# Kernel optimization log

Hardware: AMD Instinct MI355X
Metric: run time of the kernel (lower is better)

Reference implementation:

```python
import jax, jax.numpy as jnp
import numpy as np

B, IN_DIM, OUT_DIM, DEGREE = 4096, 1024, 1024, 4
LN_EPS = 1e-5


def setup_inputs() -> dict:
    key = jax.random.key(0)
    k_x, k_c = jax.random.split(key)
    x = jax.random.normal(k_x, (B, IN_DIM), dtype=jnp.float32)
    # xavier_normal_ on tensor of shape (in, out, deg+1): fan_in/fan_out from
    # torch convention: fan_in = out*(deg+1)? torch computes fan_in=size(1)*receptive,
    # for 3D tensor fan_in = shape[1]*shape[2], fan_out = shape[0]*shape[2].
    fan_in = OUT_DIM * (DEGREE + 1)
    fan_out = IN_DIM * (DEGREE + 1)
    std = float(np.sqrt(2.0 / (fan_in + fan_out)))
    cheby_coeffs = jax.random.normal(k_c, (IN_DIM, OUT_DIM, DEGREE + 1), dtype=jnp.float32) * std
    ln_weight = jnp.ones((IN_DIM,), dtype=jnp.float32)
    ln_bias = jnp.zeros((IN_DIM,), dtype=jnp.float32)
    return {"x": x, "cheby_coeffs": cheby_coeffs, "ln_weight": ln_weight, "ln_bias": ln_bias}


def _layer_norm(x, w, b):
    mu = jnp.mean(x, axis=-1, keepdims=True)
    var = jnp.mean(jnp.square(x - mu), axis=-1, keepdims=True)
    return (x - mu) * jax.lax.rsqrt(var + LN_EPS) * w + b


def reference(x, cheby_coeffs, ln_weight, ln_bias):
    h = jnp.tanh(_layer_norm(x, ln_weight, ln_bias))  # [B, I]
    # Chebyshev recurrence T0=1, T1=h, T_{n}=2h*T_{n-1}-T_{n-2}
    cheby = [jnp.ones_like(h), h]
    for _ in range(2, DEGREE + 1):
        cheby.append(2.0 * h * cheby[-1] - cheby[-2])
    stacked = jnp.stack(cheby, axis=-1)  # [B, I, D+1]
    y = jnp.einsum('bid,iod->bo', stacked, cheby_coeffs)
    return jax.nn.silu(y)
```

## Files before the change

kernel.cpp:

```cpp
#include <hip/hip_runtime.h>
#include <cstdint>
#include <cstddef>

#define BATCH 4096
#define IDIM 1024
#define ODIM 1024
#define KDIM 4096
#define KHALF 2048

typedef __attribute__((ext_vector_type(4))) int i32x4;
typedef __attribute__((ext_vector_type(16))) int i32x16;

#define CS_INV 1514.7f
#define DEQ_SCALE (6.602e-4f / 127.0f)

__device__ __forceinline__ char q8(float v, float s) {
  int i = __float2int_rn(v * s);
  i = max(-127, min(127, i));
  return (char)i;
}

__device__ __forceinline__ void load_lds16(const void* g, void* l) {
  __builtin_amdgcn_global_load_lds(
      (const __attribute__((address_space(1))) void*)g,
      (__attribute__((address_space(3))) void*)l, 16, 0, 0);
}

__global__ __launch_bounds__(256) void prep(
    const float* __restrict__ x, const float* __restrict__ lnw,
    const float* __restrict__ lnb, const float* __restrict__ C,
    char* __restrict__ A, char* __restrict__ Bq,
    float* __restrict__ bias) {
  __shared__ __align__(16) char smq[5 * 64 * 64];
  __shared__ float smf[64 * 64];
  int bid = blockIdx.x;
  int t = threadIdx.x;

  if (bid < BATCH) {
    float* rs = smf;
    float* rq = smf + 4;
    const float4 v = ((const float4*)(x + (size_t)bid * IDIM))[t];
    float s  = v.x + v.y + v.z + v.w;
    float s2 = v.x * v.x + v.y * v.y + v.z * v.z + v.w * v.w;
#pragma unroll
    for (int off = 32; off > 0; off >>= 1) {
      s  += __shfl_down(s, off);
      s2 += __shfl_down(s2, off);
    }
    int lane = t & 63, wv = t >> 6;
    if (lane == 0) { rs[wv] = s; rq[wv] = s2; }
    __syncthreads();
    float S1 = rs[0] + rs[1] + rs[2] + rs[3];
    float S2 = rq[0] + rq[1] + rq[2] + rq[3];
    float mean = S1 * (1.0f / IDIM);
    float var  = S2 * (1.0f / IDIM) - mean * mean;
    float rstd = rsqrtf(var + 1e-5f);

    const float4 w4 = ((const float4*)lnw)[t];
    const float4 b4 = ((const float4*)lnb)[t];
    float xs[4]  = {v.x, v.y, v.z, v.w};
    float ws4[4] = {w4.x, w4.y, w4.z, w4.w};
    float bs4[4] = {b4.x, b4.y, b4.z, b4.w};

    char q1[4], q2[4], q3[4], q4[4];
#pragma unroll
    for (int j = 0; j < 4; j++) {
      float h  = tanhf((xs[j] - mean) * rstd * ws4[j] + bs4[j]);
      float T2 = 2.0f * h * h - 1.0f;
      float T3 = 2.0f * h * T2 - h;
      float T4 = 2.0f * h * T3 - T2;
      q1[j] = q8(h, 127.f); q2[j] = q8(T2, 127.f);
      q3[j] = q8(T3, 127.f); q4[j] = q8(T4, 127.f);
    }
    size_t base = (size_t)bid * KDIM;
    *(uint32_t*)(A + base + 0 * IDIM + t * 4) = *(uint32_t*)q1;
    *(uint32_t*)(A + base + 1 * IDIM + t * 4) = *(uint32_t*)q2;
    *(uint32_t*)(A + base + 2 * IDIM + t * 4) = *(uint32_t*)q3;
    *(uint32_t*)(A + base + 3 * IDIM + t * 4) = *(uint32_t*)q4;
  } else {
    int cb = bid - BATCH;
    int i0 = (cb & 15) * 64, o0 = (cb >> 4) * 64;
#pragma unroll
    for (int r = 0; r < 20; r++) {
      int idx = r * 256 + t;
      int ii  = idx / 80;
      int c4  = idx - ii * 80;
      const float4 f = *(const float4*)(C + ((size_t)(i0 + ii) * ODIM + o0) * 5 + c4 * 4);
      float vals[4] = {f.x, f.y, f.z, f.w};
#pragma unroll
      for (int j = 0; j < 4; j++) {
        int p  = c4 * 4 + j;
        int oo = p / 5, d = p - oo * 5;
        if (d == 0) smf[oo * 64 + ii] = vals[j];
        else        smq[p * 64 + ((ii + 4 * p) & 63)] = q8(vals[j], CS_INV);
      }
    }
    __syncthreads();
#pragma unroll
    for (int r = 0; r < 16; r++) {
      int idx = r * 256 + t;
      int seg = idx >> 4, l16 = idx & 15;
      int oo = seg >> 2, d2 = seg & 3;
      int p = oo * 5 + d2 + 1;
      char4 u = *(const char4*)&smq[p * 64 + 4 * ((l16 + p) & 15)];
      *(char4*)(Bq + (size_t)(o0 + oo) * KDIM + d2 * IDIM + i0 + l16 * 4) = u;
    }
    if (t < 64) {
      float s = 0.f;
#pragma unroll
      for (int k = 0; k < 64; k++) s += smf[t * 64 + ((k + t) & 63)];
      atomicAdd(&bias[o0 + t], s);
    }
  }
}

#define BM 128
#define BN 128
#define BKB 128
#define NIT (KHALF / BKB)

__global__ __launch_bounds__(256, 2) void gemm_part(
    const char* __restrict__ A,
    const char* __restrict__ Bq,
    int* __restrict__ p0,
    int* __restrict__ p1) {
  __shared__ char As[2][BM * BKB];
  __shared__ char Bs[2][BN * BKB];
  int t = threadIdx.x;
  int lane = t & 63, w = t >> 6;
  int m0 = blockIdx.x * BM;
  int n0 = blockIdx.y * BN;
  size_t kbase = (size_t)blockIdx.z * KHALF;

  i32x16 acc[2][2];
#pragma unroll
  for (int i = 0; i < 2; i++)
#pragma unroll
    for (int j = 0; j < 2; j++)
#pragma unroll
      for (int r = 0; r < 16; r++) acc[i][j][r] = 0;

  int wm = (w >> 1) * 64;
  int wn = (w & 1) * 64;

  int sr = lane >> 3;
  int sc = ((lane & 7) ^ sr) * 16;
  const char* ag[4]; char* al[4];
  const char* bg[4]; char* bl[4];
#pragma unroll
  for (int q = 0; q < 4; q++) {
    int row = w * 8 + q * 32;
    ag[q] = A  + (size_t)(m0 + row + sr) * KDIM + kbase + sc;
    al[q] = &As[0][row * BKB];
    bg[q] = Bq + (size_t)(n0 + row + sr) * KDIM + kbase + sc;
    bl[q] = &Bs[0][row * BKB];
  }

  int l31 = lane & 31, hb = lane >> 5, x7 = lane & 7;
  int arow0 = (wm + l31) * BKB;
  int brow0 = (wn + l31) * BKB;

#define ISSUE(buf, kk0)                                                      \
  do {                                                                       \
    int _k = (kk0);                                                          \
    _Pragma("unroll")                                                        \
    for (int q = 0; q < 4; q++) load_lds16(ag[q] + _k, al[q] + (buf) * (BM * BKB)); \
    _Pragma("unroll")                                                        \
    for (int q = 0; q < 4; q++) load_lds16(bg[q] + _k, bl[q] + (buf) * (BN * BKB)); \
  } while (0)

#define COMPUTE(buf)                                                         \
  do {                                                                       \
    const char* asb = &As[buf][0];                                           \
    const char* bsb = &Bs[buf][0];                                           \
    _Pragma("unroll")                                                        \
    for (int ks = 0; ks < 4; ks++) {                                         \
      int co = ((2 * ks + hb) ^ x7) * 16;                                    \
      i32x4 af[2], bfv[2];                                                   \
      _Pragma("unroll")                                                      \
      for (int i = 0; i < 2; i++)                                            \
        af[i]  = *(const i32x4*)(asb + arow0 + i * 32 * BKB + co);           \
      _Pragma("unroll")                                                      \
      for (int j = 0; j < 2; j++)                                            \
        bfv[j] = *(const i32x4*)(bsb + brow0 + j * 32 * BKB + co);           \
      _Pragma("unroll")                                                      \
      for (int i = 0; i < 2; i++)                                            \
        _Pragma("unroll")                                                    \
        for (int j = 0; j < 2; j++)                                          \
          acc[i][j] = __builtin_amdgcn_mfma_i32_32x32x32_i8(                 \
              af[i], bfv[j], acc[i][j], 0, 0, 0);                            \
    }                                                                        \
  } while (0)

  ISSUE(0, 0);
  for (int it = 0; it < NIT; it += 2) {
    __syncthreads();
    if (it + 1 < NIT) ISSUE(1, (it + 1) * BKB);
    COMPUTE(0);
    __syncthreads();
    if (it + 2 < NIT) ISSUE(0, (it + 2) * BKB);
    COMPUTE(1);
  }

  int* dst = (blockIdx.z == 0) ? p0 : p1;
#pragma unroll
  for (int jj = 0; jj < 2; jj++) {
    int col = n0 + wn + jj * 32 + l31;
#pragma unroll
    for (int ii = 0; ii < 2; ii++) {
      int rbase = m0 + wm + ii * 32 + 4 * hb;
#pragma unroll
      for (int reg = 0; reg < 16; reg++) {
        int row = rbase + (reg & 3) + 8 * (reg >> 2);
        dst[(size_t)row * ODIM + col] = acc[ii][jj][reg];
      }
    }
  }
}

__global__ __launch_bounds__(256) void reduce_silu(
    const int* __restrict__ p0, const int* __restrict__ p1,
    const float* __restrict__ bias, float* __restrict__ out) {
  int idx = blockIdx.x * 256 + threadIdx.x;
  i32x4 a = ((const i32x4*)p0)[idx];
  i32x4 b = ((const i32x4*)p1)[idx];
  float4 bs = *(const float4*)&bias[(idx * 4) & (ODIM - 1)];
  float y0 = (float)(a[0] + b[0]) * DEQ_SCALE + bs.x;
  float y1 = (float)(a[1] + b[1]) * DEQ_SCALE + bs.y;
  float y2 = (float)(a[2] + b[2]) * DEQ_SCALE + bs.z;
  float y3 = (float)(a[3] + b[3]) * DEQ_SCALE + bs.w;
  float4 o;
  o.x = y0 / (1.0f + __expf(-y0));
  o.y = y1 / (1.0f + __expf(-y1));
  o.z = y2 / (1.0f + __expf(-y2));
  o.w = y3 / (1.0f + __expf(-y3));
  ((float4*)out)[idx] = o;
}

extern "C" void kernel_launch(void* const* d_in, const int* in_sizes, int n_in,
                              void* d_out, int out_size, void* d_ws, size_t ws_size,
                              hipStream_t stream) {
  const float* x    = (const float*)d_in[0];
  const float* coef = (const float*)d_in[1];
  const float* lnw  = (const float*)d_in[2];
  const float* lnb  = (const float*)d_in[3];
  float* out = (float*)d_out;

  char* ws = (char*)d_ws;
  char* A    = ws;
  char* Bq   = ws + (size_t)BATCH * KDIM;
  float* bias = (float*)(Bq + (size_t)ODIM * KDIM);
  int* p0 = (int*)((char*)bias + 65536);
  int* p1 = p0 + (size_t)BATCH * ODIM;

  hipMemsetAsync(bias, 0, ODIM * sizeof(float), stream);
  prep<<<BATCH + 256, 256, 0, stream>>>(x, lnw, lnb, coef, A, Bq, bias);
  gemm_part<<<dim3(BATCH / BM, ODIM / BN, 2), 256, 0, stream>>>(A, Bq, p0, p1);
  reduce_silu<<<(BATCH * ODIM) / (256 * 4), 256, 0, stream>>>(p0, p1, bias, out);
}
```

Measured before the change: 133.2 us.

## Load GEMM A operand straight into registers and replace bias atomics with partials

The int8 GEMM no longer stages the A tile through LDS. Each wave loads its A fragments from global memory into a double-buffered register array and feeds them to the MFMA, which halves LDS use and removes the LDS reads for A. Separately, the prep kernel writes per-input-block bias partial sums into a 16-row buffer instead of atomically adding into one bias vector. This removes the memset and the atomics, and the reduce kernel now sums the 16 partials. The trade-offs are extra VGPR pressure, duplicated A loads across waves that share rows, and less coalesced global access for A.

```diff
diff --git a/kernel.cpp b/kernel.cpp
--- a/kernel.cpp
+++ b/kernel.cpp
@@ -30,7 +30,7 @@
     const float* __restrict__ x, const float* __restrict__ lnw,
     const float* __restrict__ lnb, const float* __restrict__ C,
     char* __restrict__ A, char* __restrict__ Bq,
-    float* __restrict__ bias) {
+    float* __restrict__ biasPart) {
   __shared__ __align__(16) char smq[5 * 64 * 64];
   __shared__ float smf[64 * 64];
   int bid = blockIdx.x;
@@ -109,7 +109,7 @@
       float s = 0.f;
 #pragma unroll
       for (int k = 0; k < 64; k++) s += smf[t * 64 + ((k + t) & 63)];
-      atomicAdd(&bias[o0 + t], s);
+      biasPart[(size_t)(i0 >> 6) * ODIM + o0 + t] = s;
     }
   }
 }
@@ -124,7 +124,6 @@
     const char* __restrict__ Bq,
     int* __restrict__ p0,
     int* __restrict__ p1) {
-  __shared__ char As[2][BM * BKB];
   __shared__ char Bs[2][BN * BKB];
   int t = threadIdx.x;
   int lane = t & 63, w = t >> 6;
@@ -145,41 +144,43 @@
 
   int sr = lane >> 3;
   int sc = ((lane & 7) ^ sr) * 16;
-  const char* ag[4]; char* al[4];
   const char* bg[4]; char* bl[4];
 #pragma unroll
   for (int q = 0; q < 4; q++) {
     int row = w * 8 + q * 32;
-    ag[q] = A  + (size_t)(m0 + row + sr) * KDIM + kbase + sc;
-    al[q] = &As[0][row * BKB];
     bg[q] = Bq + (size_t)(n0 + row + sr) * KDIM + kbase + sc;
     bl[q] = &Bs[0][row * BKB];
   }
 
   int l31 = lane & 31, hb = lane >> 5, x7 = lane & 7;
-  int arow0 = (wm + l31) * BKB;
   int brow0 = (wn + l31) * BKB;
+
+  const char* ap[2];
+#pragma unroll
+  for (int i = 0; i < 2; i++)
+    ap[i] = A + (size_t)(m0 + wm + i * 32 + l31) * KDIM + kbase + hb * 16;
+
+  i32x4 afr[2][2][4];
 
 #define ISSUE(buf, kk0)                                                      \
   do {                                                                       \
     int _k = (kk0);                                                          \
     _Pragma("unroll")                                                        \
-    for (int q = 0; q < 4; q++) load_lds16(ag[q] + _k, al[q] + (buf) * (BM * BKB)); \
+    for (int q = 0; q < 4; q++) load_lds16(bg[q] + _k, bl[q] + (buf) * (BN * BKB)); \
     _Pragma("unroll")                                                        \
-    for (int q = 0; q < 4; q++) load_lds16(bg[q] + _k, bl[q] + (buf) * (BN * BKB)); \
+    for (int i = 0; i < 2; i++)                                              \
+      _Pragma("unroll")                                                      \
+      for (int ks = 0; ks < 4; ks++)                                         \
+        afr[buf][i][ks] = *(const i32x4*)(ap[i] + _k + ks * 32);             \
   } while (0)
 
 #define COMPUTE(buf)                                                         \
   do {                                                                       \
-    const char* asb = &As[buf][0];                                           \
     const char* bsb = &Bs[buf][0];                                           \
     _Pragma("unroll")                                                        \
     for (int ks = 0; ks < 4; ks++) {                                         \
       int co = ((2 * ks + hb) ^ x7) * 16;                                    \
-      i32x4 af[2], bfv[2];                                                   \
-      _Pragma("unroll")                                                      \
-      for (int i = 0; i < 2; i++)                                            \
-        af[i]  = *(const i32x4*)(asb + arow0 + i * 32 * BKB + co);           \
+      i32x4 bfv[2];                                                          \
       _Pragma("unroll")                                                      \
       for (int j = 0; j < 2; j++)                                            \
         bfv[j] = *(const i32x4*)(bsb + brow0 + j * 32 * BKB + co);           \
@@ -188,7 +189,7 @@
         _Pragma("unroll")                                                    \
         for (int j = 0; j < 2; j++)                                          \
           acc[i][j] = __builtin_amdgcn_mfma_i32_32x32x32_i8(                 \
-              af[i], bfv[j], acc[i][j], 0, 0, 0);                            \
+              afr[buf][i][ks], bfv[j], acc[i][j], 0, 0, 0);                  \
     }                                                                        \
   } while (0)
 
@@ -220,11 +221,17 @@
 
 __global__ __launch_bounds__(256) void reduce_silu(
     const int* __restrict__ p0, const int* __restrict__ p1,
-    const float* __restrict__ bias, float* __restrict__ out) {
+    const float* __restrict__ biasPart, float* __restrict__ out) {
   int idx = blockIdx.x * 256 + threadIdx.x;
   i32x4 a = ((const i32x4*)p0)[idx];
   i32x4 b = ((const i32x4*)p1)[idx];
-  float4 bs = *(const float4*)&bias[(idx * 4) & (ODIM - 1)];
+  int col0 = (idx * 4) & (ODIM - 1);
+  float4 bs = {0.f, 0.f, 0.f, 0.f};
+#pragma unroll
+  for (int ib = 0; ib < 16; ib++) {
+    float4 f = *(const float4*)&biasPart[(size_t)ib * ODIM + col0];
+    bs.x += f.x; bs.y += f.y; bs.z += f.z; bs.w += f.w;
+  }
   float y0 = (float)(a[0] + b[0]) * DEQ_SCALE + bs.x;
   float y1 = (float)(a[1] + b[1]) * DEQ_SCALE + bs.y;
   float y2 = (float)(a[2] + b[2]) * DEQ_SCALE + bs.z;
@@ -249,12 +256,11 @@
   char* ws = (char*)d_ws;
   char* A    = ws;
   char* Bq   = ws + (size_t)BATCH * KDIM;
-  float* bias = (float*)(Bq + (size_t)ODIM * KDIM);
-  int* p0 = (int*)((char*)bias + 65536);
+  float* biasPart = (float*)(Bq + (size_t)ODIM * KDIM);
+  int* p0 = (int*)((char*)biasPart + 65536);
   int* p1 = p0 + (size_t)BATCH * ODIM;
 
-  hipMemsetAsync(bias, 0, ODIM * sizeof(float), stream);
-  prep<<<BATCH + 256, 256, 0, stream>>>(x, lnw, lnb, coef, A, Bq, bias);
+  prep<<<BATCH + 256, 256, 0, stream>>>(x, lnw, lnb, coef, A, Bq, biasPart);
   gemm_part<<<dim3(BATCH / BM, ODIM / BN, 2), 256, 0, stream>>>(A, Bq, p0, p1);
-  reduce_silu<<<(BATCH * ODIM) / (256 * 4), 256, 0, stream>>>(p0, p1, bias, out);
-}
+  reduce_silu<<<(BATCH * ODIM) / (256 * 4), 256, 0, stream>>>(p0, p1, biasPart, out);
+}
```

Measured after the change: 152.4 us. 1.14x slower.
